# Performance work log

Hardware: AMD Instinct MI355X
Metric: run time of the kernel (lower is better)

## Reference

```python
import jax, jax.numpy as jnp
import numpy as np


def setup_inputs() -> dict:
    key = jax.random.key(0)
    ks = jax.random.split(key, 5)
    B, Lq, Lkv, HQ, H, D, S, BS = 1, 256, 4096, 32, 2, 128, 16, 64
    q = jax.random.normal(ks[0], (B, Lq, HQ, D), jnp.float32)
    k = jax.random.normal(ks[1], (B, Lkv, H, D), jnp.float32)
    v = jax.random.normal(ks[2], (B, Lkv, H, D), jnp.float32)
    w = jax.random.uniform(ks[3], (B, Lq, HQ, S), jnp.float32)
    block_indices = jax.random.randint(ks[4], (B, Lq, H, S), 0, Lkv // BS).astype(jnp.int32)
    return {"q": q, "k": k, "v": v, "w": w, "block_indices": block_indices, "block_size": BS}


def reference(q, k, v, w, block_indices, block_size):
    # q: (B, Lq, HQ, D); k,v: (B, Lkv, H, D); w: (B, Lq, HQ, num_weights);
    # block_indices: (B, Lq, H, S) int32, entries < 0 are skipped.
    B, Lq, HQ, D = q.shape
    H = k.shape[2]
    S = block_indices.shape[-1]
    G = HQ // H  # query heads per kv head
    nb = k.shape[1] // block_size
    sm_scale = 1.0 / (D ** 0.5)  # default scale in the kernel

    # Reshape KV into blocks: (B, H, nb, BS, D)
    kb = k.reshape(B, nb, block_size, H, D).transpose(0, 3, 1, 2, 4)
    vb = v.reshape(B, nb, block_size, H, D).transpose(0, 3, 1, 2, 4)

    idx = block_indices.transpose(0, 2, 1, 3)  # (B, H, Lq, S)
    valid = idx >= 0
    idx = jnp.maximum(idx, 0)

    # Gather selected blocks per (batch, kv_head): -> (B, H, Lq, S, BS, D)
    gather = jax.vmap(jax.vmap(lambda blocks, ind: blocks[ind]))
    kg = gather(kb, idx)
    vg = gather(vb, idx)

    # Group query heads by kv head: (B, H, Lq, G, D)
    qh = q.reshape(B, Lq, H, G, D).transpose(0, 2, 1, 3, 4)

    # Per-block scores and per-block softmax over the BS keys (axis u)
    scores = jnp.einsum('bhlgd,bhlsud->bhlgsu', qh, kg) * sm_scale
    p = jax.nn.softmax(scores, axis=-1)

    # Per-(head, block) learned weight; only first S weights of w are used.
    wh = w[..., :S].reshape(B, Lq, H, G, S).transpose(0, 2, 1, 3, 4)  # (B,H,Lq,G,S)
    coef = wh * valid[:, :, :, None, :].astype(p.dtype)
    p = p * coef[..., None]

    o = jnp.einsum('bhlgsu,bhlsud->bhlgd', p, vg)  # (B, H, Lq, G, D)
    return o.transpose(0, 2, 1, 3, 4).reshape(B, Lq, HQ, D)
```

## Files before the change

### kernel.cpp

```cpp
#include <hip/hip_runtime.h>
#include <hip/hip_bf16.h>


namespace {

constexpr int kLq = 256, kHQ = 32, kH = 2, kG = 16, kD = 128, kS = 16;
constexpr int kNB = 64;
constexpr float kScaleLog2e = 0.08838834764831845f * 1.4426950408889634f;

constexpr int kKPackN = kH * kNB * 16 * 64;
constexpr int kPStr   = 72;
constexpr int kSStr   = 136;

typedef short s16x8 __attribute__((ext_vector_type(8)));
typedef float f32x4 __attribute__((ext_vector_type(4)));

union U32BF2 { unsigned int u; __hip_bfloat162 h; };
union FragU  { uint4 u; s16x8 v; };

static __device__ inline unsigned int pk_bf16(float a, float b) {
    U32BF2 z; z.h = __float22bfloat162_rn(make_float2(a, b));
    return z.u;
}

__global__ __launch_bounds__(256)
void pack_kv(const float* __restrict__ k, const float* __restrict__ v,
             uint4* __restrict__ kp, uint4* __restrict__ vp)
{
    __shared__ unsigned short S_s[32 * kSStr];

    const int bid  = blockIdx.x;
    const int isV  = bid & 1;
    const int half = (bid >> 1) & 1;
    const int blk  = (bid >> 2) & 63;
    const int h    = bid >> 8;
    const int t    = threadIdx.x;
    const int lane = t & 63, n = lane & 15, quad = lane >> 4;
    const int wv   = t >> 6;

    {
        const float* src = (isV ? v : k) +
            ((size_t)(blk * 64 + half * 32) * kH + h) * kD;
        const int r0 = t >> 5, c4 = (t & 31) << 2;
        #pragma unroll
        for (int p = 0; p < 4; ++p) {
            const int r = p * 8 + r0;
            const float4 f = *(const float4*)(src + (size_t)r * (kH * kD) + c4);
            *(unsigned int*)&S_s[r * kSStr + c4]     = pk_bf16(f.x, f.y);
            *(unsigned int*)&S_s[r * kSStr + c4 + 2] = pk_bf16(f.z, f.w);
        }
    }
    __syncthreads();

    const size_t obase = (size_t)(h * 64 + blk) * 16 * 64;
    if (!isV) {
        #pragma unroll
        for (int rep = 0; rep < 2; ++rep) {
            const int cl    = wv * 2 + rep;
            const int t_loc = cl >> 2, st = cl & 3;
            const int c     = (2 * half + t_loc) * 4 + st;
            const int u_loc = t_loc * 16 + n;
            kp[obase + (size_t)c * 64 + lane] =
                *(const uint4*)&S_s[u_loc * kSStr + st * 32 + quad * 8];
        }
    } else {
        #pragma unroll
        for (int rep = 0; rep < 2; ++rep) {
            const int dt = wv * 2 + rep;
            const int c  = dt * 2 + half;
            const int d  = dt * 16 + n;
            unsigned short s[8];
            #pragma unroll
            for (int j = 0; j < 8; ++j) s[j] = S_s[(quad * 8 + j) * kSStr + d];
            uint4 val;
            val.x = s[0] | ((unsigned)s[1] << 16);
            val.y = s[2] | ((unsigned)s[3] << 16);
            val.z = s[4] | ((unsigned)s[5] << 16);
            val.w = s[6] | ((unsigned)s[7] << 16);
            vp[obase + (size_t)c * 64 + lane] = val;
        }
    }
}

__global__ __launch_bounds__(256, 3)
void hsa_main(const float* __restrict__ q, const float* __restrict__ w,
              const int* __restrict__ bidx, const uint4* __restrict__ kp,
              const uint4* __restrict__ vp, float* __restrict__ out)
{
    __shared__ __align__(16) uint4 vbuf[2][16 * 64];
    __shared__ __align__(16) unsigned short P_s[2][kG * kPStr];
    __shared__ __align__(16) float psum[2][kG][4];

    const int bid  = blockIdx.x;
    const int l    = bid >> 1;
    const int h    = bid & 1;
    const int tid  = threadIdx.x;
    const int wave = tid >> 6;
    const int lane = tid & 63;
    const int n    = lane & 15;
    const int quad = lane >> 4;

    s16x8 qf[4];
    {
        const float* qb = q + ((size_t)l * kHQ + h * kG + n) * kD + quad * 8;
        #pragma unroll
        for (int st = 0; st < 4; ++st) {
            const float4 f0 = *(const float4*)(qb + st * 32);
            const float4 f1 = *(const float4*)(qb + st * 32 + 4);
            union { s16x8 v; unsigned int u[4]; } z;
            z.u[0] = pk_bf16(f0.x, f0.y); z.u[1] = pk_bf16(f0.z, f0.w);
            z.u[2] = pk_bf16(f1.x, f1.y); z.u[3] = pk_bf16(f1.z, f1.w);
            qf[st] = z.v;
        }
    }

    int   base_[kS];
    float wval[kS];
    #pragma unroll
    for (int i = 0; i < 4; ++i) {
        const int4   b4 = *(const int4*)(bidx + (size_t)(l * kH + h) * kS + i * 4);
        const float4 w4 = *(const float4*)(w + ((size_t)l * kHQ + h * kG + n) * kS + i * 4);
        const int   bb[4] = {b4.x, b4.y, b4.z, b4.w};
        const float ww[4] = {w4.x, w4.y, w4.z, w4.w};
        #pragma unroll
        for (int jj = 0; jj < 4; ++jj) {
            wval[i * 4 + jj]  = (bb[jj] < 0) ? 0.f : ww[jj];
            base_[i * 4 + jj] = (h * kNB + max(bb[jj], 0)) * 1024;
        }
    }

    #define STAGE_V(js_, b_)                                                   \
        {                                                                      \
            const uint4* gp = vp + base_[(js_)] + (wave * 4) * 64 + lane;      \
            auto* lp = (__attribute__((address_space(3))) uint4*)              \
                           &vbuf[(b_)][(wave * 4) * 64];                       \
            _Pragma("unroll")                                                  \
            for (int i_ = 0; i_ < 4; ++i_)                                     \
                __builtin_amdgcn_global_load_lds(                              \
                    (const __attribute__((address_space(1))) void*)(gp + i_ * 64), \
                    (__attribute__((address_space(3))) void*)(lp + i_ * 64),   \
                    16, 0, 0);                                                 \
        }

    STAGE_V(0, 0);
    FragU kreg[4];
    #pragma unroll
    for (int st = 0; st < 4; ++st)
        kreg[st].u = kp[base_[0] + (wave * 4 + st) * 64 + lane];
    __builtin_amdgcn_sched_barrier(0);

    f32x4 oacc0 = {0.f, 0.f, 0.f, 0.f};
    f32x4 oacc1 = {0.f, 0.f, 0.f, 0.f};

    #pragma unroll
    for (int js = 0; js < kS; ++js) {
        const int cur = js & 1;

        f32x4 sc = {0.f, 0.f, 0.f, 0.f};
        #pragma unroll
        for (int st = 0; st < 4; ++st)
            sc = __builtin_amdgcn_mfma_f32_16x16x32_bf16(kreg[st].v, qf[st], sc, 0, 0, 0);

        if (js < kS - 1) {
            #pragma unroll
            for (int st = 0; st < 4; ++st)
                kreg[st].u = kp[base_[js + 1] + (wave * 4 + st) * 64 + lane];
        }
        __builtin_amdgcn_sched_barrier(0);

        float part = 0.f;
        #pragma unroll
        for (int r = 0; r < 4; ++r) {
            sc[r] = exp2f(sc[r] * kScaleLog2e);
            part += sc[r];
        }
        part += __shfl_xor(part, 16);
        part += __shfl_xor(part, 32);
        if (quad == 0) psum[cur][n][wave] = part;

        const unsigned long long pq =
            ((unsigned long long)pk_bf16(sc[2], sc[3]) << 32) | pk_bf16(sc[0], sc[1]);
        *(unsigned long long*)&P_s[cur][n * kPStr + wave * 16 + quad * 4] = pq;

        __syncthreads();

        const float4 ps  = *(const float4*)&psum[cur][n][0];
        const float coef = wval[js] / (ps.x + ps.y + ps.z + ps.w);
        const s16x8 bf0 = *(const s16x8*)&P_s[cur][n * kPStr + quad * 8];
        const s16x8 bf1 = *(const s16x8*)&P_s[cur][n * kPStr + 32 + quad * 8];

        if (js < kS - 1) { STAGE_V(js + 1, cur ^ 1); }
        __builtin_amdgcn_sched_barrier(0);

        const f32x4 zero = {0.f, 0.f, 0.f, 0.f};
        const s16x8 a0 = *(const s16x8*)&vbuf[cur][(wave * 4 + 0) * 64 + lane];
        const s16x8 a1 = *(const s16x8*)&vbuf[cur][(wave * 4 + 1) * 64 + lane];
        const s16x8 a2 = *(const s16x8*)&vbuf[cur][(wave * 4 + 2) * 64 + lane];
        const s16x8 a3 = *(const s16x8*)&vbuf[cur][(wave * 4 + 3) * 64 + lane];
        f32x4 p0 = __builtin_amdgcn_mfma_f32_16x16x32_bf16(a0, bf0, zero, 0, 0, 0);
        p0       = __builtin_amdgcn_mfma_f32_16x16x32_bf16(a1, bf1, p0,   0, 0, 0);
        f32x4 p1 = __builtin_amdgcn_mfma_f32_16x16x32_bf16(a2, bf0, zero, 0, 0, 0);
        p1       = __builtin_amdgcn_mfma_f32_16x16x32_bf16(a3, bf1, p1,   0, 0, 0);
        #pragma unroll
        for (int r = 0; r < 4; ++r) {
            oacc0[r] = fmaf(coef, p0[r], oacc0[r]);
            oacc1[r] = fmaf(coef, p1[r], oacc1[r]);
        }
    }
    #undef STAGE_V

    {
        float* ob = out + ((size_t)l * kHQ + h * kG + n) * kD;
        const int d0 = wave * 32 + quad * 4;
        *(float4*)(ob + d0)      = make_float4(oacc0[0], oacc0[1], oacc0[2], oacc0[3]);
        *(float4*)(ob + d0 + 16) = make_float4(oacc1[0], oacc1[1], oacc1[2], oacc1[3]);
    }
}

}

extern "C" void kernel_launch(void* const* d_in, const int* in_sizes, int n_in,
                              void* d_out, int out_size, void* d_ws, size_t ws_size,
                              hipStream_t stream)
{
    const float* q    = (const float*)d_in[0];
    const float* k    = (const float*)d_in[1];
    const float* v    = (const float*)d_in[2];
    const float* w    = (const float*)d_in[3];
    const int*   bidx = (const int*)d_in[4];
    float* out = (float*)d_out;

    uint4* kp = (uint4*)d_ws;
    uint4* vp = (uint4*)((char*)d_ws + (size_t)kKPackN * 16);

    pack_kv<<<dim3(512), dim3(256), 0, stream>>>(k, v, kp, vp);
    hsa_main<<<dim3(kLq * kH), dim3(256), 0, stream>>>(q, w, bidx, kp, vp, out);
}
```

Before: 97.12 us.

## Split selected blocks across two wave teams and reduce partial outputs in LDS

Each workgroup now runs 512 threads as two teams of four waves. Each team processes alternating selected KV blocks (8 each instead of 16 sequentially), and the two partial output accumulators are summed through LDS at the end. The K register prefetch is moved after the barrier, next to the V staging. This halves the serial loop length per workgroup to expose more parallelism, at the cost of double the LDS footprint, an extra reduction barrier, and possibly lower occupancy.

Result: faster. 93.83 us (-3.4%).

```diff
diff --git a/kernel.cpp b/kernel.cpp
--- a/kernel.cpp
+++ b/kernel.cpp
@@ -82,20 +82,22 @@
     }
 }
 
-__global__ __launch_bounds__(256, 3)
+__global__ __launch_bounds__(512, 4)
 void hsa_main(const float* __restrict__ q, const float* __restrict__ w,
               const int* __restrict__ bidx, const uint4* __restrict__ kp,
               const uint4* __restrict__ vp, float* __restrict__ out)
 {
-    __shared__ __align__(16) uint4 vbuf[2][16 * 64];
-    __shared__ __align__(16) unsigned short P_s[2][kG * kPStr];
-    __shared__ __align__(16) float psum[2][kG][4];
+    __shared__ __align__(16) uint4 vbuf[2][2][16 * 64];
+    __shared__ __align__(16) unsigned short P_s[2][2][kG * kPStr];
+    __shared__ __align__(16) float psum[2][2][kG][4];
 
     const int bid  = blockIdx.x;
     const int l    = bid >> 1;
     const int h    = bid & 1;
     const int tid  = threadIdx.x;
     const int wave = tid >> 6;
+    const int team = wave >> 2;
+    const int tw   = wave & 3;
     const int lane = tid & 63;
     const int n    = lane & 15;
     const int quad = lane >> 4;
@@ -114,26 +116,21 @@
         }
     }
 
-    int   base_[kS];
-    float wval[kS];
+    int   base8[8];
+    float wval8[8];
     #pragma unroll
-    for (int i = 0; i < 4; ++i) {
-        const int4   b4 = *(const int4*)(bidx + (size_t)(l * kH + h) * kS + i * 4);
-        const float4 w4 = *(const float4*)(w + ((size_t)l * kHQ + h * kG + n) * kS + i * 4);
-        const int   bb[4] = {b4.x, b4.y, b4.z, b4.w};
-        const float ww[4] = {w4.x, w4.y, w4.z, w4.w};
-        #pragma unroll
-        for (int jj = 0; jj < 4; ++jj) {
-            wval[i * 4 + jj]  = (bb[jj] < 0) ? 0.f : ww[jj];
-            base_[i * 4 + jj] = (h * kNB + max(bb[jj], 0)) * 1024;
-        }
-    }
-
-    #define STAGE_V(js_, b_)                                                   \
+    for (int j = 0; j < 8; ++j) {
+        const int s  = 2 * j + team;
+        const int bi = bidx[(size_t)(l * kH + h) * kS + s];
+        wval8[j] = (bi < 0) ? 0.f : w[((size_t)l * kHQ + h * kG + n) * kS + s];
+        base8[j] = (h * kNB + max(bi, 0)) * 1024;
+    }
+
+    #define STAGE_V(jp_, b_)                                                   \
         {                                                                      \
-            const uint4* gp = vp + base_[(js_)] + (wave * 4) * 64 + lane;      \
+            const uint4* gp = vp + base8[(jp_)] + (tw * 4) * 64 + lane;        \
             auto* lp = (__attribute__((address_space(3))) uint4*)              \
-                           &vbuf[(b_)][(wave * 4) * 64];                       \
+                           &vbuf[(b_)][team][(tw * 4) * 64];                   \
             _Pragma("unroll")                                                  \
             for (int i_ = 0; i_ < 4; ++i_)                                     \
                 __builtin_amdgcn_global_load_lds(                              \
@@ -146,27 +143,20 @@
     FragU kreg[4];
     #pragma unroll
     for (int st = 0; st < 4; ++st)
-        kreg[st].u = kp[base_[0] + (wave * 4 + st) * 64 + lane];
+        kreg[st].u = kp[base8[0] + (tw * 4 + st) * 64 + lane];
     __builtin_amdgcn_sched_barrier(0);
 
     f32x4 oacc0 = {0.f, 0.f, 0.f, 0.f};
     f32x4 oacc1 = {0.f, 0.f, 0.f, 0.f};
 
     #pragma unroll
-    for (int js = 0; js < kS; ++js) {
-        const int cur = js & 1;
+    for (int jp = 0; jp < 8; ++jp) {
+        const int cur = jp & 1;
 
         f32x4 sc = {0.f, 0.f, 0.f, 0.f};
         #pragma unroll
         for (int st = 0; st < 4; ++st)
             sc = __builtin_amdgcn_mfma_f32_16x16x32_bf16(kreg[st].v, qf[st], sc, 0, 0, 0);
-
-        if (js < kS - 1) {
-            #pragma unroll
-            for (int st = 0; st < 4; ++st)
-                kreg[st].u = kp[base_[js + 1] + (wave * 4 + st) * 64 + lane];
-        }
-        __builtin_amdgcn_sched_barrier(0);
 
         float part = 0.f;
         #pragma unroll
@@ -176,27 +166,32 @@
         }
         part += __shfl_xor(part, 16);
         part += __shfl_xor(part, 32);
-        if (quad == 0) psum[cur][n][wave] = part;
+        if (quad == 0) psum[cur][team][n][tw] = part;
 
         const unsigned long long pq =
             ((unsigned long long)pk_bf16(sc[2], sc[3]) << 32) | pk_bf16(sc[0], sc[1]);
-        *(unsigned long long*)&P_s[cur][n * kPStr + wave * 16 + quad * 4] = pq;
+        *(unsigned long long*)&P_s[cur][team][n * kPStr + tw * 16 + quad * 4] = pq;
 
         __syncthreads();
 
-        const float4 ps  = *(const float4*)&psum[cur][n][0];
-        const float coef = wval[js] / (ps.x + ps.y + ps.z + ps.w);
-        const s16x8 bf0 = *(const s16x8*)&P_s[cur][n * kPStr + quad * 8];
-        const s16x8 bf1 = *(const s16x8*)&P_s[cur][n * kPStr + 32 + quad * 8];
-
-        if (js < kS - 1) { STAGE_V(js + 1, cur ^ 1); }
+        if (jp < 7) {
+            #pragma unroll
+            for (int st = 0; st < 4; ++st)
+                kreg[st].u = kp[base8[jp + 1] + (tw * 4 + st) * 64 + lane];
+            STAGE_V(jp + 1, cur ^ 1);
+        }
         __builtin_amdgcn_sched_barrier(0);
 
+        const float4 ps  = *(const float4*)&psum[cur][team][n][0];
+        const float coef = wval8[jp] / (ps.x + ps.y + ps.z + ps.w);
+        const s16x8 bf0 = *(const s16x8*)&P_s[cur][team][n * kPStr + quad * 8];
+        const s16x8 bf1 = *(const s16x8*)&P_s[cur][team][n * kPStr + 32 + quad * 8];
+
         const f32x4 zero = {0.f, 0.f, 0.f, 0.f};
-        const s16x8 a0 = *(const s16x8*)&vbuf[cur][(wave * 4 + 0) * 64 + lane];
-        const s16x8 a1 = *(const s16x8*)&vbuf[cur][(wave * 4 + 1) * 64 + lane];
-        const s16x8 a2 = *(const s16x8*)&vbuf[cur][(wave * 4 + 2) * 64 + lane];
-        const s16x8 a3 = *(const s16x8*)&vbuf[cur][(wave * 4 + 3) * 64 + lane];
+        const s16x8 a0 = *(const s16x8*)&vbuf[cur][team][(tw * 4 + 0) * 64 + lane];
+        const s16x8 a1 = *(const s16x8*)&vbuf[cur][team][(tw * 4 + 1) * 64 + lane];
+        const s16x8 a2 = *(const s16x8*)&vbuf[cur][team][(tw * 4 + 2) * 64 + lane];
+        const s16x8 a3 = *(const s16x8*)&vbuf[cur][team][(tw * 4 + 3) * 64 + lane];
         f32x4 p0 = __builtin_amdgcn_mfma_f32_16x16x32_bf16(a0, bf0, zero, 0, 0, 0);
         p0       = __builtin_amdgcn_mfma_f32_16x16x32_bf16(a1, bf1, p0,   0, 0, 0);
         f32x4 p1 = __builtin_amdgcn_mfma_f32_16x16x32_bf16(a2, bf0, zero, 0, 0, 0);
@@ -209,11 +204,29 @@
     }
     #undef STAGE_V
 
+    __syncthreads();
     {
-        float* ob = out + ((size_t)l * kHQ + h * kG + n) * kD;
-        const int d0 = wave * 32 + quad * 4;
-        *(float4*)(ob + d0)      = make_float4(oacc0[0], oacc0[1], oacc0[2], oacc0[3]);
-        *(float4*)(ob + d0 + 16) = make_float4(oacc1[0], oacc1[1], oacc1[2], oacc1[3]);
+        float* Ored = (float*)&vbuf[0][0][0];
+        if (team == 1) {
+            #pragma unroll
+            for (int r = 0; r < 4; ++r) {
+                Ored[((tw * 2 + 0) * 16 + quad * 4 + r) * 16 + n] = oacc0[r];
+                Ored[((tw * 2 + 1) * 16 + quad * 4 + r) * 16 + n] = oacc1[r];
+            }
+        }
+        __syncthreads();
+        if (team == 0) {
+            float* ob = out + ((size_t)l * kHQ + h * kG + n) * kD;
+            const int d0 = tw * 32 + quad * 4;
+            float4 v0, v1;
+            #pragma unroll
+            for (int r = 0; r < 4; ++r) {
+                (&v0.x)[r] = oacc0[r] + Ored[(d0 + r) * 16 + n];
+                (&v1.x)[r] = oacc1[r] + Ored[(d0 + 16 + r) * 16 + n];
+            }
+            *(float4*)(ob + d0)      = v0;
+            *(float4*)(ob + d0 + 16) = v1;
+        }
     }
 }
 
@@ -234,5 +247,5 @@
     uint4* vp = (uint4*)((char*)d_ws + (size_t)kKPackN * 16);
 
     pack_kv<<<dim3(512), dim3(256), 0, stream>>>(k, v, kp, vp);
-    hsa_main<<<dim3(kLq * kH), dim3(256), 0, stream>>>(q, w, bidx, kp, vp, out);
-}
+    hsa_main<<<dim3(kLq * kH), dim3(512), 0, stream>>>(q, w, bidx, kp, vp, out);
+}
```
